# Kernel tuning notes

Measured on AMD Instinct MI355X. Metric: run time of the kernel, lower is better.

The kernel has to match this reference:

```python
import jax, jax.numpy as jnp
import numpy as np

TOPK = 8
N_EXPERTS = 64
ROUTE_SCALE = 1.0


def setup_inputs() -> dict:
    key = jax.random.key(0)
    k1, k2 = jax.random.split(key)
    x = jax.random.normal(k1, (16, 256, 64, 64), dtype=jnp.float32)
    gate_w = jax.random.normal(k2, (64, 256, 3, 3), dtype=jnp.float32) * 0.02  # [E, C, kh, kw]
    bias = jnp.zeros((64,), dtype=jnp.float32)  # load-balancing bias buffer
    return {"x": x, "gate_w": gate_w, "bias": bias}


def reference(x, gate_w, bias):
    # 3x3 conv, stride 1, pad 1 (SAME), no conv bias -> expert logits [B, E, H, W]
    logits = jax.lax.conv_general_dilated(
        x, gate_w, window_strides=(1, 1), padding="SAME",
        dimension_numbers=("NCHW", "OIHW", "NCHW"))
    scores = jax.nn.sigmoid(logits)                 # [B, E, H, W]
    s = jnp.moveaxis(scores, 1, -1)                 # [B, H, W, E]
    biased = s + bias                               # bias broadcast over experts
    _, idx = jax.lax.top_k(biased, TOPK)            # [B, H, W, K] (topk on biased scores)
    w = jnp.take_along_axis(s, idx, axis=-1)        # gather UNbiased scores
    w = jax.nn.softmax(w, axis=-1) * ROUTE_SCALE    # softmax over the K selected experts
    weights = jnp.moveaxis(w, -1, 1)                # [B, K, H, W] to match torch layout
    indices = jnp.moveaxis(idx, -1, 1)              # [B, K, H, W]
    counts = jnp.zeros((N_EXPERTS,), jnp.int32).at[idx.ravel()].add(1)  # bincount
    return weights, indices, counts
```

## Files before the change

### kernel.cpp

```cpp
#include <hip/hip_runtime.h>


typedef _Float16 half8 __attribute__((ext_vector_type(8)));
typedef __attribute__((ext_vector_type(4))) float f32x4;

#define LOG2E 1.44269504f

__device__ __forceinline__ unsigned short f2h_bits(float f) {
    _Float16 h = (_Float16)f;
    unsigned short b;
    __builtin_memcpy(&b, &h, 2);
    return b;
}

constexpr int WB_U4 = 8 * 9 * 4 * 64;

__global__ __launch_bounds__(256) void gate_prep(const float* __restrict__ gw,
                                                 unsigned short* __restrict__ wB) {
    int g = blockIdx.x * 256 + threadIdx.x;
    if (g >= WB_U4) return;
    int lane = g & 63;
    int nt   = (g >> 6) & 3;
    int rest = g >> 8;
    int t = rest % 9, q = rest / 9;
    int e  = nt * 16 + (lane & 15);
    int c0 = q * 32 + (lane >> 4) * 8;
    unsigned short o[8];
#pragma unroll
    for (int j = 0; j < 8; ++j)
        o[j] = f2h_bits(gw[(e * 256 + c0 + j) * 9 + t]);
    uint4 pk;
    pk.x = (unsigned)o[0] | ((unsigned)o[1] << 16);
    pk.y = (unsigned)o[2] | ((unsigned)o[3] << 16);
    pk.z = (unsigned)o[4] | ((unsigned)o[5] << 16);
    pk.w = (unsigned)o[6] | ((unsigned)o[7] << 16);
    ((uint4*)wB)[g] = pk;
}

constexpr int CSTR  = 40;
constexpr int SSTR  = 68;
constexpr int SCF_B = 64 * SSTR * 4;

__global__ __launch_bounds__(256, 4) void gate_main(
    const float* __restrict__ x, const float* __restrict__ bias,
    const unsigned short* __restrict__ wB, float* __restrict__ out) {
    __shared__ unsigned char smem[SCF_B + 512];
    unsigned short* xs     = (unsigned short*)smem;
    float*          scf    = (float*)smem;
    float*          bias_s = (float*)(smem + SCF_B);
    int*            hist   = (int*)(smem + SCF_B + 256);

    const int tid  = threadIdx.x;
    const int lane = tid & 63;
    const int rw   = tid >> 6;
    const int blk  = blockIdx.x;
    const int b    = blk & 15;
    const int r    = blk >> 4;

    if (tid < 64) { bias_s[tid] = bias[tid]; hist[tid] = 0; }

    const int  r0   = tid >> 6;
    const int  w_   = tid & 63;
    const bool smain = (tid < 192);
    const int  gr   = r - 1 + r0;
    const bool rok  = smain && (gr >= 0) && (gr < 64);
    const float* xbase = x + (((size_t)(b * 256) * 64 + gr) * 64 + w_);
    unsigned short* sdst = xs + (r0 * 66 + (w_ + 1)) * CSTR;

    auto stage = [&](int q) {
        if (smain) {
            const float* p = xbase + (size_t)q * 32 * 4096;
            if (rok) {
#pragma unroll
                for (int bt = 0; bt < 4; ++bt) {
                    float v0 = p[(bt*8+0)*4096], v1 = p[(bt*8+1)*4096];
                    float v2 = p[(bt*8+2)*4096], v3 = p[(bt*8+3)*4096];
                    float v4 = p[(bt*8+4)*4096], v5 = p[(bt*8+5)*4096];
                    float v6 = p[(bt*8+6)*4096], v7 = p[(bt*8+7)*4096];
                    uint4 pk;
                    pk.x = (unsigned)f2h_bits(v0) | ((unsigned)f2h_bits(v1) << 16);
                    pk.y = (unsigned)f2h_bits(v2) | ((unsigned)f2h_bits(v3) << 16);
                    pk.z = (unsigned)f2h_bits(v4) | ((unsigned)f2h_bits(v5) << 16);
                    pk.w = (unsigned)f2h_bits(v6) | ((unsigned)f2h_bits(v7) << 16);
                    *(uint4*)(sdst + bt * 8) = pk;
                }
            } else {
                uint4 z = {0, 0, 0, 0};
#pragma unroll
                for (int bt = 0; bt < 4; ++bt) *(uint4*)(sdst + bt * 8) = z;
            }
        } else if (tid < 192 + 24) {
            int idx = tid - 192;
            int hr = idx >> 3, hc = (idx >> 2) & 1, hg = idx & 3;
            uint4 z = {0, 0, 0, 0};
            *(uint4*)(xs + (hr * 66 + hc * 65) * CSTR + hg * 8) = z;
        }
    };

    const int ph = rw >> 1;
    const int eh = rw & 1;

    f32x4 acc[2][2];
#pragma unroll
    for (int mt = 0; mt < 2; ++mt)
#pragma unroll
        for (int nt = 0; nt < 2; ++nt) acc[mt][nt] = (f32x4){0.f, 0.f, 0.f, 0.f};

#pragma unroll 1
    for (int q = 0; q < 8; ++q) {
        uint4 Bf[18];
#pragma unroll
        for (int t = 0; t < 9; ++t)
#pragma unroll
            for (int ntl = 0; ntl < 2; ++ntl)
                Bf[t * 2 + ntl] = ((const uint4*)wB)
                    [((q * 9 + t) * 4 + eh * 2 + ntl) * 64 + lane];

        __syncthreads();
        stage(q);
        __syncthreads();

#pragma unroll
        for (int t = 0; t < 9; ++t) {
            const int kh = t / 3, kw = t % 3;
            const unsigned short* abase =
                xs + (kh * 66 + kw + ph * 32 + (lane & 15)) * CSTR + (lane >> 4) * 8;
            half8 afr[2];
#pragma unroll
            for (int mt = 0; mt < 2; ++mt)
                afr[mt] = *(const half8*)(abase + mt * 16 * CSTR);
#pragma unroll
            for (int ntl = 0; ntl < 2; ++ntl) {
                half8 bfr;
                __builtin_memcpy(&bfr, &Bf[t * 2 + ntl], 16);
#pragma unroll
                for (int mt = 0; mt < 2; ++mt)
                    acc[mt][ntl] = __builtin_amdgcn_mfma_f32_16x16x32_f16(
                        afr[mt], bfr, acc[mt][ntl], 0, 0, 0);
            }
        }
    }

    __syncthreads();
#pragma unroll
    for (int mt = 0; mt < 2; ++mt)
#pragma unroll
        for (int nt = 0; nt < 2; ++nt)
#pragma unroll
            for (int rr = 0; rr < 4; ++rr) {
                float v = acc[mt][nt][rr];
                float s = 1.f / (1.f + __builtin_amdgcn_exp2f(-v * LOG2E));
                int p = ph * 32 + mt * 16 + ((lane >> 4) << 2) + rr;
                int e = eh * 32 + nt * 16 + (lane & 15);
                scf[p * SSTR + e] = s;
            }
    __syncthreads();

    if (tid < 64) {
        const float* row = scf + tid * SSTR;
        float tv[8];
        int   ti[8];
#pragma unroll
        for (int k = 0; k < 8; ++k) { tv[k] = -3.0e38f; ti[k] = 0; }
#pragma unroll
        for (int j4 = 0; j4 < 16; ++j4) {
            f32x4 blkv = *(const f32x4*)(row + j4 * 4);
#pragma unroll
            for (int j = 0; j < 4; ++j) {
                int   e  = j4 * 4 + j;
                float bs = blkv[j] + bias_s[e];
                if (bs > tv[7]) {
                    tv[7] = bs; ti[7] = e;
#pragma unroll
                    for (int k = 7; k > 0; --k) {
                        float fa = tv[k - 1], fb = tv[k];
                        int   ia = ti[k - 1], ib = ti[k];
                        bool  sw = fb > fa;
                        tv[k - 1] = sw ? fb : fa; tv[k] = sw ? fa : fb;
                        ti[k - 1] = sw ? ib : ia; ti[k] = sw ? ia : ib;
                    }
                }
            }
        }
        float u[8], mx = -3.0e38f;
#pragma unroll
        for (int k = 0; k < 8; ++k) { u[k] = tv[k] - bias_s[ti[k]]; mx = fmaxf(mx, u[k]); }
        float ex[8], sum = 0.f;
#pragma unroll
        for (int k = 0; k < 8; ++k) { ex[k] = __builtin_amdgcn_exp2f((u[k] - mx) * LOG2E); sum += ex[k]; }
        float inv = 1.f / sum;

        int obase = b * 32768 + r * 64 + tid;
#pragma unroll
        for (int k = 0; k < 8; ++k) {
            out[obase + k * 4096]          = ex[k] * inv;
            out[524288 + obase + k * 4096] = (float)ti[k];
            atomicAdd(&hist[ti[k]], 1);
        }
    }
    __syncthreads();
    if (tid < 64) atomicAdd(out + 1048576 + tid, (float)hist[tid]);
}

extern "C" void kernel_launch(void* const* d_in, const int* in_sizes, int n_in,
                              void* d_out, int out_size, void* d_ws, size_t ws_size,
                              hipStream_t stream) {
    const float* x    = (const float*)d_in[0];
    const float* gw   = (const float*)d_in[1];
    const float* bias = (const float*)d_in[2];
    float* out = (float*)d_out;
    unsigned short* wB = (unsigned short*)d_ws;

    hipMemsetAsync((char*)d_out + (size_t)1048576 * sizeof(float), 0,
                   64 * sizeof(float), stream);
    gate_prep<<<72, 256, 0, stream>>>(gw, wB);
    gate_main<<<1024, 256, 0, stream>>>(x, bias, wB, out);
}
```

Measured before the change: 167.3 us.

## Double-buffer input slab and software-pipeline weight/activation fragment loads

Replaces the single shared-memory staging buffer with two slabs, so the global loads for the next channel group are issued during the MFMA loop of the current group and committed partway through. The per-tap A and B fragments are prefetched through a three-slot register rotation instead of loading all 18 weight fragments up front. The staging work is spread over all 256 threads including the halo, and the counts memset is folded into the prep kernel to drop one launch. This is meant to hide global load latency and cut barriers, at the cost of doubling LDS use (about 32KB per block), which may reduce occupancy under the 4-block launch bound.

```diff
diff --git a/kernel.cpp b/kernel.cpp
--- a/kernel.cpp
+++ b/kernel.cpp
@@ -16,8 +16,10 @@
 constexpr int WB_U4 = 8 * 9 * 4 * 64;
 
 __global__ __launch_bounds__(256) void gate_prep(const float* __restrict__ gw,
-                                                 unsigned short* __restrict__ wB) {
+                                                 unsigned short* __restrict__ wB,
+                                                 float* __restrict__ out) {
     int g = blockIdx.x * 256 + threadIdx.x;
+    if (blockIdx.x == 0 && threadIdx.x < 64) out[1048576 + threadIdx.x] = 0.f;
     if (g >= WB_U4) return;
     int lane = g & 63;
     int nt   = (g >> 6) & 3;
@@ -37,18 +39,16 @@
     ((uint4*)wB)[g] = pk;
 }
 
-constexpr int CSTR  = 40;
-constexpr int SSTR  = 68;
-constexpr int SCF_B = 64 * SSTR * 4;
+constexpr int CSTR = 40;
+constexpr int SLAB = 3 * 66 * CSTR;
+constexpr int SSTR = 68;
 
 __global__ __launch_bounds__(256, 4) void gate_main(
     const float* __restrict__ x, const float* __restrict__ bias,
     const unsigned short* __restrict__ wB, float* __restrict__ out) {
-    __shared__ unsigned char smem[SCF_B + 512];
-    unsigned short* xs     = (unsigned short*)smem;
-    float*          scf    = (float*)smem;
-    float*          bias_s = (float*)(smem + SCF_B);
-    int*            hist   = (int*)(smem + SCF_B + 256);
+    __shared__ unsigned short xs[2 * SLAB];
+    __shared__ float bias_s[64];
+    __shared__ int   hist[64];
 
     const int tid  = threadIdx.x;
     const int lane = tid & 63;
@@ -59,89 +59,108 @@
 
     if (tid < 64) { bias_s[tid] = bias[tid]; hist[tid] = 0; }
 
-    const int  r0   = tid >> 6;
-    const int  w_   = tid & 63;
-    const bool smain = (tid < 192);
-    const int  gr   = r - 1 + r0;
-    const bool rok  = smain && (gr >= 0) && (gr < 64);
-    const float* xbase = x + (((size_t)(b * 256) * 64 + gr) * 64 + w_);
-    unsigned short* sdst = xs + (r0 * 66 + (w_ + 1)) * CSTR;
-
-    auto stage = [&](int q) {
-        if (smain) {
-            const float* p = xbase + (size_t)q * 32 * 4096;
-            if (rok) {
-#pragma unroll
-                for (int bt = 0; bt < 4; ++bt) {
-                    float v0 = p[(bt*8+0)*4096], v1 = p[(bt*8+1)*4096];
-                    float v2 = p[(bt*8+2)*4096], v3 = p[(bt*8+3)*4096];
-                    float v4 = p[(bt*8+4)*4096], v5 = p[(bt*8+5)*4096];
-                    float v6 = p[(bt*8+6)*4096], v7 = p[(bt*8+7)*4096];
-                    uint4 pk;
-                    pk.x = (unsigned)f2h_bits(v0) | ((unsigned)f2h_bits(v1) << 16);
-                    pk.y = (unsigned)f2h_bits(v2) | ((unsigned)f2h_bits(v3) << 16);
-                    pk.z = (unsigned)f2h_bits(v4) | ((unsigned)f2h_bits(v5) << 16);
-                    pk.w = (unsigned)f2h_bits(v6) | ((unsigned)f2h_bits(v7) << 16);
-                    *(uint4*)(sdst + bt * 8) = pk;
-                }
-            } else {
-                uint4 z = {0, 0, 0, 0};
-#pragma unroll
-                for (int bt = 0; bt < 4; ++bt) *(uint4*)(sdst + bt * 8) = z;
-            }
-        } else if (tid < 192 + 24) {
-            int idx = tid - 192;
-            int hr = idx >> 3, hc = (idx >> 2) & 1, hg = idx & 3;
-            uint4 z = {0, 0, 0, 0};
-            *(uint4*)(xs + (hr * 66 + hc * 65) * CSTR + hg * 8) = z;
-        }
-    };
-
-    const int ph = rw >> 1;
-    const int eh = rw & 1;
+    bool tEx[4], tOk[4];
+    int  tSrc[4], tDst[4];
+#pragma unroll
+    for (int i = 0; i < 4; ++i) {
+        int T = tid + i * 256;
+        tEx[i] = (T < 792);
+        int chh = T / 198, s = T - chh * 198;
+        int row2 = s / 66, wp = s - row2 * 66;
+        int gr = r - 1 + row2, gwc = wp - 1;
+        tOk[i]  = tEx[i] && (gr >= 0) && (gr < 64) && (gwc >= 0) && (gwc < 64);
+        tSrc[i] = ((b * 256 + chh * 8) * 64 + gr) * 64 + gwc;
+        tDst[i] = (row2 * 66 + wp) * CSTR + chh * 8;
+    }
+
+    float tb0[8], tb1[8];
+    auto issue = [&](int i, int q, float* tb) {
+        if (tOk[i]) {
+            const float* p = x + tSrc[i] + q * 131072;
+#pragma unroll
+            for (int u = 0; u < 8; ++u) tb[u] = p[u * 4096];
+        } else {
+#pragma unroll
+            for (int u = 0; u < 8; ++u) tb[u] = 0.f;
+        }
+    };
+    auto commit = [&](int i, const float* tb, unsigned short* dst) {
+        if (tEx[i]) {
+            uint4 pk;
+            pk.x = (unsigned)f2h_bits(tb[0]) | ((unsigned)f2h_bits(tb[1]) << 16);
+            pk.y = (unsigned)f2h_bits(tb[2]) | ((unsigned)f2h_bits(tb[3]) << 16);
+            pk.z = (unsigned)f2h_bits(tb[4]) | ((unsigned)f2h_bits(tb[5]) << 16);
+            pk.w = (unsigned)f2h_bits(tb[6]) | ((unsigned)f2h_bits(tb[7]) << 16);
+            *(uint4*)(dst + tDst[i]) = pk;
+        }
+    };
+
+    const int ph = rw >> 1, eh = rw & 1;
+    half8 Aa[3][2];
+    uint4 Bb[3][2];
+    auto prefA = [&](const unsigned short* buf, int t, int slot) {
+        const int kh = t / 3, kw = t % 3;
+        const unsigned short* abase =
+            buf + (kh * 66 + ph * 32 + (lane & 15) + kw) * CSTR + (lane >> 4) * 8;
+#pragma unroll
+        for (int mt = 0; mt < 2; ++mt)
+            Aa[slot][mt] = *(const half8*)(abase + mt * 16 * CSTR);
+    };
+    auto prefB = [&](int q, int t, int slot) {
+        const uint4* bp = (const uint4*)wB + ((q * 9 + t) * 4 + eh * 2) * 64 + lane;
+#pragma unroll
+        for (int nt = 0; nt < 2; ++nt) Bb[slot][nt] = bp[nt * 64];
+    };
 
     f32x4 acc[2][2];
 #pragma unroll
     for (int mt = 0; mt < 2; ++mt)
 #pragma unroll
         for (int nt = 0; nt < 2; ++nt) acc[mt][nt] = (f32x4){0.f, 0.f, 0.f, 0.f};
+
+    auto mfma_tap = [&](int slot) {
+#pragma unroll
+        for (int nt = 0; nt < 2; ++nt) {
+            half8 bfr;
+            __builtin_memcpy(&bfr, &Bb[slot][nt], 16);
+#pragma unroll
+            for (int mt = 0; mt < 2; ++mt)
+                acc[mt][nt] = __builtin_amdgcn_mfma_f32_16x16x32_f16(
+                    Aa[slot][mt], bfr, acc[mt][nt], 0, 0, 0);
+        }
+    };
+
+    issue(0, 0, tb0); issue(1, 0, tb1);
+    commit(0, tb0, xs); commit(1, tb1, xs);
+    issue(2, 0, tb0); issue(3, 0, tb1);
+    commit(2, tb0, xs); commit(3, tb1, xs);
+    __syncthreads();
 
 #pragma unroll 1
     for (int q = 0; q < 8; ++q) {
-        uint4 Bf[18];
-#pragma unroll
-        for (int t = 0; t < 9; ++t)
-#pragma unroll
-            for (int ntl = 0; ntl < 2; ++ntl)
-                Bf[t * 2 + ntl] = ((const uint4*)wB)
-                    [((q * 9 + t) * 4 + eh * 2 + ntl) * 64 + lane];
-
+        const unsigned short* cur = xs + (q & 1) * SLAB;
+        unsigned short*       nxt = xs + ((q + 1) & 1) * SLAB;
+        const bool st = (q < 7);
+        if (st) { issue(0, q + 1, tb0); issue(1, q + 1, tb1); }
+        prefA(cur, 0, 0); prefB(q, 0, 0);
+        prefA(cur, 1, 1); prefB(q, 1, 1); mfma_tap(0);
+        prefA(cur, 2, 2); prefB(q, 2, 2); mfma_tap(1);
+        prefA(cur, 3, 0); prefB(q, 3, 0); mfma_tap(2);
+        prefA(cur, 4, 1); prefB(q, 4, 1); mfma_tap(0);
+        if (st) {
+            commit(0, tb0, nxt); commit(1, tb1, nxt);
+            issue(2, q + 1, tb0); issue(3, q + 1, tb1);
+        }
+        prefA(cur, 5, 2); prefB(q, 5, 2); mfma_tap(1);
+        prefA(cur, 6, 0); prefB(q, 6, 0); mfma_tap(2);
+        prefA(cur, 7, 1); prefB(q, 7, 1); mfma_tap(0);
+        prefA(cur, 8, 2); prefB(q, 8, 2); mfma_tap(1);
+        mfma_tap(2);
+        if (st) { commit(2, tb0, nxt); commit(3, tb1, nxt); }
         __syncthreads();
-        stage(q);
-        __syncthreads();
-
-#pragma unroll
-        for (int t = 0; t < 9; ++t) {
-            const int kh = t / 3, kw = t % 3;
-            const unsigned short* abase =
-                xs + (kh * 66 + kw + ph * 32 + (lane & 15)) * CSTR + (lane >> 4) * 8;
-            half8 afr[2];
-#pragma unroll
-            for (int mt = 0; mt < 2; ++mt)
-                afr[mt] = *(const half8*)(abase + mt * 16 * CSTR);
-#pragma unroll
-            for (int ntl = 0; ntl < 2; ++ntl) {
-                half8 bfr;
-                __builtin_memcpy(&bfr, &Bf[t * 2 + ntl], 16);
-#pragma unroll
-                for (int mt = 0; mt < 2; ++mt)
-                    acc[mt][ntl] = __builtin_amdgcn_mfma_f32_16x16x32_f16(
-                        afr[mt], bfr, acc[mt][ntl], 0, 0, 0);
-            }
-        }
     }
 
-    __syncthreads();
+    float* scf = (float*)xs;
 #pragma unroll
     for (int mt = 0; mt < 2; ++mt)
 #pragma unroll
@@ -211,8 +230,6 @@
     float* out = (float*)d_out;
     unsigned short* wB = (unsigned short*)d_ws;
 
-    hipMemsetAsync((char*)d_out + (size_t)1048576 * sizeof(float), 0,
-                   64 * sizeof(float), stream);
-    gate_prep<<<72, 256, 0, stream>>>(gw, wB);
+    gate_prep<<<72, 256, 0, stream>>>(gw, wB, out);
     gate_main<<<1024, 256, 0, stream>>>(x, bias, wB, out);
 }
```

Result: faster. 153.3 us (-8.4%).
